# Optimization experiments

Measured on AMD Instinct MI355X. Metric: run time of the kernel, lower is better.

Reference implementation:

```python
import jax, jax.numpy as jnp
import numpy as np

B, S, D = 64, 1024, 256
N_HEADS = 1
HEAD_DIM = D // N_HEADS
MASK_VAL = -10000.0


def setup_inputs() -> dict:
    key = jax.random.key(0)
    k1, k2, k3 = jax.random.split(key, 3)
    x = jax.random.normal(k1, (B, S, D), dtype=jnp.float32)
    W_qkv = jax.random.normal(k2, (D, 3 * D), dtype=jnp.float32) * 0.02
    b_qkv = jnp.zeros((3 * D,), dtype=jnp.float32)
    W_out = jax.random.normal(k3, (D, D), dtype=jnp.float32) * 0.02
    b_out = jnp.zeros((D,), dtype=jnp.float32)
    return {"x": x, "W_qkv": W_qkv, "b_qkv": b_qkv, "W_out": W_out, "b_out": b_out}


def reference(x, W_qkv, b_qkv, W_out, b_out):
    # QKV projection: [B,S,3D]
    qkv = jnp.einsum('bsd,df->bsf', x, W_qkv) + b_qkv
    q, k, v = jnp.split(qkv, 3, axis=2)
    # split heads -> [B,H,S,hd] (H=1)
    def split_heads(t):
        return t.reshape(B, S, N_HEADS, HEAD_DIM).transpose(0, 2, 1, 3)
    q, k, v = split_heads(q), split_heads(k), split_heads(v)
    # scaled scores [B,H,S,S]
    scores = jnp.einsum('bhqd,bhkd->bhqk', q, k) / jnp.sqrt(jnp.float32(HEAD_DIM))
    causal = jnp.tril(jnp.ones((1, 1, S, S), dtype=bool))
    scores = jnp.where(causal, scores, jnp.float32(MASK_VAL))
    attn = jax.nn.softmax(scores, axis=-1)  # dropout deterministic (training=False)
    out = jnp.einsum('bhqk,bhkd->bhqd', attn, v)
    # merge heads -> [B,S,D]
    out = out.transpose(0, 2, 1, 3).reshape(B, S, D)
    out = jnp.einsum('bsd,de->bse', out, W_out) + b_out
    return out, attn
```

## Files before the change

kernel.cpp:

```cpp
#include <hip/hip_runtime.h>
#include <hip/hip_bf16.h>

#define BB 64
#define SS 1024
#define DDIM 256

typedef unsigned short u16;
typedef __attribute__((ext_vector_type(4))) float f4;
typedef __attribute__((ext_vector_type(8))) short bf16x8;
typedef __attribute__((ext_vector_type(4))) short bf16x4;
typedef __attribute__((ext_vector_type(4))) float f32x4;

__device__ inline u16 f2b(float f) {
  unsigned int u = __float_as_uint(f);
  unsigned int r = (u + 0x7fffu + ((u >> 16) & 1u)) >> 16;
  return (u16)r;
}

#define GLOAD16(g, l)                                                  \
  __builtin_amdgcn_global_load_lds(                                    \
      (const __attribute__((address_space(1))) void*)(g),              \
      (__attribute__((address_space(3))) void*)(l), 16, 0, 0)

__global__ __launch_bounds__(256) void cast_x(const float* __restrict__ x,
                                              u16* __restrict__ xb, int n8) {
  int i = blockIdx.x * 256 + threadIdx.x;
  const int stride = gridDim.x * 256;
  for (; i < n8; i += stride) {
    f4 a = ((const f4*)x)[2 * i];
    f4 b = ((const f4*)x)[2 * i + 1];
    bf16x8 o;
    o[0] = f2b(a[0]); o[1] = f2b(a[1]); o[2] = f2b(a[2]); o[3] = f2b(a[3]);
    o[4] = f2b(b[0]); o[5] = f2b(b[1]); o[6] = f2b(b[2]); o[7] = f2b(b[3]);
    ((bf16x8*)xb)[i] = o;
  }
}

__global__ __launch_bounds__(256) void cast_w(const float* __restrict__ Wqkv,
                                              const float* __restrict__ Wout,
                                              u16* __restrict__ Wqkvt,
                                              u16* __restrict__ Woutt) {
  int t = blockIdx.x * 256 + threadIdx.x;
  if (t < 256 * 768) {
    int k = t / 768, n = t % 768;
    Wqkvt[n * 256 + k] = f2b(Wqkv[t]);
  }
  if (t < 256 * 256) {
    int k = t / 256, n = t % 256;
    Woutt[n * 256 + k] = f2b(Wout[t]);
  }
}

template <int EPI, int NXT>
__global__ __launch_bounds__(256) void gemm_mfma(
    const u16* __restrict__ A, const u16* __restrict__ Bt,
    const float* __restrict__ bias, float* __restrict__ outF,
    u16* __restrict__ Qb, u16* __restrict__ Kb, u16* __restrict__ Vt) {
  __shared__ u16 As[128 * 64];
  __shared__ u16 Bs[128 * 64];
  const int t = threadIdx.x;
  const int w = t >> 6, l = t & 63;
  const int lr = l & 15, lg = l >> 4;
  const int id = blockIdx.x;
  const int r8 = id & 7;
  const int tt = id >> 3;
  const int xt = tt % NXT;
  const int yt = (tt / NXT) * 8 + r8;
  const int m0 = yt * 128, n0 = xt * 128;
  const int wm = (w >> 1) * 64, wn = (w & 1) * 64;

  f32x4 acc[4][4] = {};

  const int srow = w * 8 + (l >> 3);
  const int csrc = (l & 7) ^ (srow & 7);

  for (int k0 = 0; k0 < 256; k0 += 64) {
    __syncthreads();
#pragma unroll
    for (int i = 0; i < 4; ++i) {
      const int row = i * 32 + srow;
      GLOAD16(&A[(size_t)(m0 + row) * 256 + k0 + csrc * 8],
              &As[(i * 32 + w * 8) * 64]);
      GLOAD16(&Bt[(size_t)(n0 + row) * 256 + k0 + csrc * 8],
              &Bs[(i * 32 + w * 8) * 64]);
    }
    __syncthreads();
#pragma unroll
    for (int kc = 0; kc < 2; ++kc) {
      bf16x8 af[4], bfr[4];
#pragma unroll
      for (int f = 0; f < 4; ++f) {
        int ar = wm + f * 16 + lr;
        af[f] = *(const bf16x8*)&As[ar * 64 + (((kc * 4 + lg) ^ (ar & 7)) * 8)];
        int br = wn + f * 16 + lr;
        bfr[f] = *(const bf16x8*)&Bs[br * 64 + (((kc * 4 + lg) ^ (br & 7)) * 8)];
      }
#pragma unroll
      for (int i = 0; i < 4; ++i)
#pragma unroll
        for (int jn = 0; jn < 4; ++jn)
          acc[i][jn] = __builtin_amdgcn_mfma_f32_16x16x32_bf16(
              af[i], bfr[jn], acc[i][jn], 0, 0, 0);
    }
  }

#pragma unroll
  for (int i = 0; i < 4; ++i) {
    const int mbase = m0 + wm + i * 16 + lg * 4;
#pragma unroll
    for (int jn = 0; jn < 4; ++jn) {
      const int n = n0 + wn + jn * 16 + lr;
      const float bv = bias[n];
      if (EPI == 0) {
#pragma unroll
        for (int r = 0; r < 4; ++r)
          outF[(size_t)(mbase + r) * 256 + n] = acc[i][jn][r] + bv;
      } else {
        if (n < 256) {
#pragma unroll
          for (int r = 0; r < 4; ++r)
            Qb[(size_t)(mbase + r) * 256 + n] = f2b(acc[i][jn][r] + bv);
        } else if (n < 512) {
#pragma unroll
          for (int r = 0; r < 4; ++r)
            Kb[(size_t)(mbase + r) * 256 + (n - 256)] = f2b(acc[i][jn][r] + bv);
        } else {
          const int d = n - 512;
          const int b = mbase >> 10, sl = mbase & 1023;
          bf16x4 pk;
#pragma unroll
          for (int r = 0; r < 4; ++r) pk[r] = f2b(acc[i][jn][r] + bv);
          *(bf16x4*)&Vt[((size_t)b * 256 + d) * 1024 + sl] = pk;
        }
      }
    }
  }
}

__global__ __launch_bounds__(256) void attn_fused(
    const u16* __restrict__ Qg, const u16* __restrict__ Kg,
    const u16* __restrict__ Vtg, float* __restrict__ attn,
    u16* __restrict__ outa) {
  __shared__ u16 pool[35328];
  u16* Ks = pool;
  u16* Vs = pool + 16384;
  u16* Ps = pool + 32768;

  const int t = threadIdx.x;
  const int w = t >> 6, l = t & 63;
  const int lr = l & 15, lg = l >> 4;
  const int id = blockIdx.x;
  const int b = (id & 7) * 8 + ((id >> 3) & 7);
  const int pair = id >> 6;
  const int qta = pair, qtb = 15 - pair;
  const int d0w = w * 64;

  const u16* Kbase = Kg + (size_t)b * SS * DDIM;
  const u16* Vbase = Vtg + (size_t)b * DDIM * SS;

  auto stageK = [&](int kt, int buf) {
    const int rbase = 8 * w;
#pragma unroll
    for (int i = 0; i < 4; ++i) {
      const int rr = rbase + 2 * i + (l >> 5);
      const int chunk = l & 31;
      const int csrc = (chunk & 24) | ((chunk & 7) ^ (rr & 7));
      const u16* g = Kbase + (size_t)(kt * 32 + rr) * DDIM + csrc * 8;
      GLOAD16(g, Ks + buf * 8192 + (rbase + 2 * i) * 256);
    }
  };
  auto stageV = [&](int kt, int buf) {
    const int dbase = 64 * w;
#pragma unroll
    for (int i = 0; i < 4; ++i) {
      const int dd = dbase + 16 * i + (l >> 2);
      const u16* g = Vbase + (size_t)dd * SS + kt * 32 + (l & 3) * 8;
      GLOAD16(g, Vs + buf * 8192 + (dbase + 16 * i) * 32);
    }
  };
  auto loadQ = [&](int qt, bf16x8* qf) {
    const u16* qb = Qg + ((size_t)(b * SS + qt * 64 + w * 16 + lr)) * DDIM;
#pragma unroll
    for (int kc = 0; kc < 8; ++kc)
      qf[kc] = *(const bf16x8*)&qb[kc * 32 + lg * 8];
  };

  bf16x8 qfA[8], qfB[8];
  loadQ(qta, qfA);
  loadQ(qtb, qfB);
  const int lastA = 2 * qta + 1, lastB = 2 * qtb + 1;
  float raA[4] = {0.f, 0.f, 0.f, 0.f}, raB[4] = {0.f, 0.f, 0.f, 0.f};

  stageK(0, 0);
  __syncthreads();
  for (int kt = 0; kt <= lastB; ++kt) {
    const int buf = kt & 1;
    if (kt < lastB) stageK(kt + 1, buf ^ 1);
    const bool doA = (kt <= lastA);
#pragma unroll
    for (int sf = 0; sf < 2; ++sf) {
      const int srow = sf * 16 + lr;
      const u16* kr = Ks + buf * 8192 + srow * 256;
      f32x4 sA = {0.f, 0.f, 0.f, 0.f}, sB = {0.f, 0.f, 0.f, 0.f};
#pragma unroll
      for (int kc = 0; kc < 8; ++kc) {
        const int c = kc * 4 + lg;
        const int ch = (c & 24) | ((c & 7) ^ (srow & 7));
        bf16x8 bfr = *(const bf16x8*)&kr[ch * 8];
        sB = __builtin_amdgcn_mfma_f32_16x16x32_bf16(qfB[kc], bfr, sB, 0, 0, 0);
        if (doA)
          sA = __builtin_amdgcn_mfma_f32_16x16x32_bf16(qfA[kc], bfr, sA, 0, 0, 0);
      }
      const int scol = kt * 32 + sf * 16 + lr;
      {
        const int qrow = qtb * 64 + w * 16 + lg * 4;
#pragma unroll
        for (int r = 0; r < 4; ++r)
          raB[r] += (scol <= qrow + r) ? __expf(sB[r] * 0.0625f) : 0.f;
      }
      if (doA) {
        const int qrow = qta * 64 + w * 16 + lg * 4;
#pragma unroll
        for (int r = 0; r < 4; ++r)
          raA[r] += (scol <= qrow + r) ? __expf(sA[r] * 0.0625f) : 0.f;
      }
    }
    __syncthreads();
  }
#pragma unroll
  for (int m = 1; m < 16; m <<= 1) {
#pragma unroll
    for (int r = 0; r < 4; ++r) {
      raA[r] += __shfl_xor(raA[r], m, 64);
      raB[r] += __shfl_xor(raB[r], m, 64);
    }
  }
  float invA[4], invB[4];
#pragma unroll
  for (int r = 0; r < 4; ++r) {
    invA[r] = 1.0f / raA[r];
    invB[r] = 1.0f / raB[r];
  }

  for (int tile = 0; tile < 2; ++tile) {
    const int qt = tile ? qtb : qta;
    const int last = 2 * qt + 1;
    bf16x8 qf[8];
    loadQ(qt, qf);
    float inv[4];
#pragma unroll
    for (int r = 0; r < 4; ++r) inv[r] = tile ? invB[r] : invA[r];
    f32x4 oacc[4][4];
#pragma unroll
    for (int qb = 0; qb < 4; ++qb)
#pragma unroll
      for (int df = 0; df < 4; ++df) oacc[qb][df] = (f32x4){0.f, 0.f, 0.f, 0.f};

    float* attnw = attn + ((size_t)(b * SS + qt * 64 + w * 16)) * SS;

    __syncthreads();
    stageK(0, 0);
    stageV(0, 0);
    __syncthreads();

    for (int kt = 0; kt <= last; ++kt) {
      const int buf = kt & 1;
#pragma unroll
      for (int sf = 0; sf < 2; ++sf) {
        const int srow = sf * 16 + lr;
        const u16* kr = Ks + buf * 8192 + srow * 256;
        f32x4 s = {0.f, 0.f, 0.f, 0.f};
#pragma unroll
        for (int kc = 0; kc < 8; ++kc) {
          const int c = kc * 4 + lg;
          const int ch = (c & 24) | ((c & 7) ^ (srow & 7));
          bf16x8 bfr = *(const bf16x8*)&kr[ch * 8];
          s = __builtin_amdgcn_mfma_f32_16x16x32_bf16(qf[kc], bfr, s, 0, 0, 0);
        }
        const int scol = kt * 32 + sf * 16 + lr;
        const int qrow = qt * 64 + w * 16 + lg * 4;
#pragma unroll
        for (int r = 0; r < 4; ++r) {
          const float e = (scol <= qrow + r) ? __expf(s[r] * 0.0625f) : 0.f;
          Ps[(w * 16 + lg * 4 + r) * 40 + sf * 16 + lr] = f2b(e * inv[r]);
        }
      }
#pragma unroll
      for (int g2 = 0; g2 < 2; ++g2) {
        const int row = g2 * 8 + (l >> 3);
        const int col = (l & 7) * 4;
        bf16x4 pv = *(const bf16x4*)&Ps[(w * 16 + row) * 40 + col];
        f4 o;
#pragma unroll
        for (int j = 0; j < 4; ++j)
          o[j] = __uint_as_float(((unsigned)(u16)pv[j]) << 16);
        *(f4*)&attnw[(size_t)row * SS + kt * 32 + col] = o;
      }
      __syncthreads();
      if (kt < last) {
        stageK(kt + 1, buf ^ 1);
        stageV(kt + 1, buf ^ 1);
      }
      bf16x8 vfr[4];
      const u16* vb = Vs + buf * 8192;
#pragma unroll
      for (int df = 0; df < 4; ++df)
        vfr[df] = *(const bf16x8*)&vb[(d0w + df * 16 + lr) * 32 + lg * 8];
#pragma unroll
      for (int qb = 0; qb < 4; ++qb) {
        bf16x8 pa = *(const bf16x8*)&Ps[(qb * 16 + lr) * 40 + lg * 8];
#pragma unroll
        for (int df = 0; df < 4; ++df)
          oacc[qb][df] = __builtin_amdgcn_mfma_f32_16x16x32_bf16(
              pa, vfr[df], oacc[qb][df], 0, 0, 0);
      }
      __syncthreads();
    }

    {
      const f4 z = {0.f, 0.f, 0.f, 0.f};
      for (int c0 = (qt + 1) * 64; c0 < SS; c0 += 32) {
#pragma unroll
        for (int g2 = 0; g2 < 2; ++g2) {
          const int row = g2 * 8 + (l >> 3);
          *(f4*)&attnw[(size_t)row * SS + c0 + (l & 7) * 4] = z;
        }
      }
    }

#pragma unroll
    for (int qb = 0; qb < 4; ++qb)
#pragma unroll
      for (int df = 0; df < 4; ++df)
#pragma unroll
        for (int r = 0; r < 4; ++r)
          pool[(qb * 16 + lg * 4 + r) * 264 + d0w + df * 16 + lr] =
              f2b(oacc[qb][df][r]);
    __syncthreads();
    {
      const size_t obase = (size_t)(b * SS + qt * 64);
#pragma unroll
      for (int i = 0; i < 8; ++i) {
        const int row = w * 16 + 2 * i + (l >> 5);
        bf16x8 v = *(const bf16x8*)&pool[row * 264 + (l & 31) * 8];
        *(bf16x8*)&outa[(obase + row) * DDIM + (l & 31) * 8] = v;
      }
    }
  }
}

extern "C" void kernel_launch(void* const* d_in, const int* in_sizes, int n_in,
                              void* d_out, int out_size, void* d_ws,
                              size_t ws_size, hipStream_t stream) {
  const float* x    = (const float*)d_in[0];
  const float* Wqkv = (const float*)d_in[1];
  const float* bqkv = (const float*)d_in[2];
  const float* Wout = (const float*)d_in[3];
  const float* bout = (const float*)d_in[4];

  float* out  = (float*)d_out;
  float* attn = out + (size_t)BB * SS * DDIM;

  const size_t NTOK = (size_t)BB * SS;
  u16* ws = (u16*)d_ws;
  u16* xb    = ws;
  u16* Qb    = xb + NTOK * DDIM;
  u16* Kb    = Qb + NTOK * DDIM;
  u16* Vt    = Kb + NTOK * DDIM;
  u16* outa  = Vt + NTOK * DDIM;
  u16* Wqkvt = outa + NTOK * DDIM;
  u16* Woutt = Wqkvt + 768 * 256;

  cast_x<<<2048, 256, 0, stream>>>(x, xb, (int)(NTOK * DDIM / 8));
  cast_w<<<768, 256, 0, stream>>>(Wqkv, Wout, Wqkvt, Woutt);

  gemm_mfma<1, 6><<<3072, 256, 0, stream>>>(xb, Wqkvt, bqkv, nullptr, Qb, Kb,
                                            Vt);
  attn_fused<<<512, 256, 0, stream>>>(Qb, Kb, Vt, attn, outa);
  gemm_mfma<0, 2><<<1024, 256, 0, stream>>>(outa, Woutt, bout, out, nullptr,
                                            nullptr, nullptr);
}
```

Baseline: 266.8 us.

## Load V fragments directly from global and cut LDS for higher occupancy

Drops the V staging buffer in LDS and has each wave read its V fragments straight from global memory into registers. This roughly halves the kernel's shared memory, and launch bounds now ask for 3 blocks per CU. The __syncthreads calls are replaced with explicit vmcnt/lgkmcnt waits, raw s_barrier and sched_barrier, so each iteration needs fewer full barriers and the next K tile is staged earlier. The risks are uncoalesced strided global reads for V, register limits under the tighter launch bound, and correctness that now depends on hand-counted vmcnt values.

```diff
diff --git a/kernel.cpp b/kernel.cpp
--- a/kernel.cpp
+++ b/kernel.cpp
@@ -21,6 +21,12 @@
   __builtin_amdgcn_global_load_lds(                                    \
       (const __attribute__((address_space(1))) void*)(g),              \
       (__attribute__((address_space(3))) void*)(l), 16, 0, 0)
+
+#define WAITVM0 asm volatile("s_waitcnt vmcnt(0)" ::: "memory")
+#define WAITVM6 asm volatile("s_waitcnt vmcnt(6)" ::: "memory")
+#define LGKM0 asm volatile("s_waitcnt lgkmcnt(0)" ::: "memory")
+#define SBAR __builtin_amdgcn_s_barrier()
+#define SCHED0 __builtin_amdgcn_sched_barrier(0)
 
 __global__ __launch_bounds__(256) void cast_x(const float* __restrict__ x,
                                               u16* __restrict__ xb, int n8) {
@@ -137,14 +143,13 @@
   }
 }
 
-__global__ __launch_bounds__(256) void attn_fused(
+__global__ __launch_bounds__(256, 3) void attn_fused(
     const u16* __restrict__ Qg, const u16* __restrict__ Kg,
     const u16* __restrict__ Vtg, float* __restrict__ attn,
     u16* __restrict__ outa) {
-  __shared__ u16 pool[35328];
+  __shared__ u16 pool[18944];
   u16* Ks = pool;
-  u16* Vs = pool + 16384;
-  u16* Ps = pool + 32768;
+  u16* Ps = pool + 16384;
 
   const int t = threadIdx.x;
   const int w = t >> 6, l = t & 63;
@@ -169,15 +174,6 @@
       GLOAD16(g, Ks + buf * 8192 + (rbase + 2 * i) * 256);
     }
   };
-  auto stageV = [&](int kt, int buf) {
-    const int dbase = 64 * w;
-#pragma unroll
-    for (int i = 0; i < 4; ++i) {
-      const int dd = dbase + 16 * i + (l >> 2);
-      const u16* g = Vbase + (size_t)dd * SS + kt * 32 + (l & 3) * 8;
-      GLOAD16(g, Vs + buf * 8192 + (dbase + 16 * i) * 32);
-    }
-  };
   auto loadQ = [&](int qt, bf16x8* qf) {
     const u16* qb = Qg + ((size_t)(b * SS + qt * 64 + w * 16 + lr)) * DDIM;
 #pragma unroll
@@ -192,9 +188,11 @@
   float raA[4] = {0.f, 0.f, 0.f, 0.f}, raB[4] = {0.f, 0.f, 0.f, 0.f};
 
   stageK(0, 0);
-  __syncthreads();
   for (int kt = 0; kt <= lastB; ++kt) {
     const int buf = kt & 1;
+    WAITVM0;
+    SBAR;
+    SCHED0;
     if (kt < lastB) stageK(kt + 1, buf ^ 1);
     const bool doA = (kt <= lastA);
 #pragma unroll
@@ -225,8 +223,8 @@
           raA[r] += (scol <= qrow + r) ? __expf(sA[r] * 0.0625f) : 0.f;
       }
     }
-    __syncthreads();
-  }
+  }
+  SBAR;
 #pragma unroll
   for (int m = 1; m < 16; m <<= 1) {
 #pragma unroll
@@ -258,13 +256,20 @@
 
     float* attnw = attn + ((size_t)(b * SS + qt * 64 + w * 16)) * SS;
 
-    __syncthreads();
     stageK(0, 0);
-    stageV(0, 0);
-    __syncthreads();
+    WAITVM0;
 
     for (int kt = 0; kt <= last; ++kt) {
       const int buf = kt & 1;
+      bf16x8 vfr[4];
+#pragma unroll
+      for (int df = 0; df < 4; ++df)
+        vfr[df] = *(const bf16x8*)&Vbase[(size_t)(d0w + df * 16 + lr) * SS +
+                                         kt * 32 + lg * 8];
+      WAITVM6;
+      SBAR;
+      SCHED0;
+      if (kt < last) stageK(kt + 1, buf ^ 1);
 #pragma unroll
       for (int sf = 0; sf < 2; ++sf) {
         const int srow = sf * 16 + lr;
@@ -296,16 +301,9 @@
           o[j] = __uint_as_float(((unsigned)(u16)pv[j]) << 16);
         *(f4*)&attnw[(size_t)row * SS + kt * 32 + col] = o;
       }
-      __syncthreads();
-      if (kt < last) {
-        stageK(kt + 1, buf ^ 1);
-        stageV(kt + 1, buf ^ 1);
-      }
-      bf16x8 vfr[4];
-      const u16* vb = Vs + buf * 8192;
-#pragma unroll
-      for (int df = 0; df < 4; ++df)
-        vfr[df] = *(const bf16x8*)&vb[(d0w + df * 16 + lr) * 32 + lg * 8];
+      LGKM0;
+      SBAR;
+      SCHED0;
 #pragma unroll
       for (int qb = 0; qb < 4; ++qb) {
         bf16x8 pa = *(const bf16x8*)&Ps[(qb * 16 + lr) * 40 + lg * 8];
@@ -314,8 +312,8 @@
           oacc[qb][df] = __builtin_amdgcn_mfma_f32_16x16x32_bf16(
               pa, vfr[df], oacc[qb][df], 0, 0, 0);
       }
-      __syncthreads();
-    }
+    }
+    SBAR;
 
     {
       const f4 z = {0.f, 0.f, 0.f, 0.f};
@@ -336,7 +334,8 @@
         for (int r = 0; r < 4; ++r)
           pool[(qb * 16 + lg * 4 + r) * 264 + d0w + df * 16 + lr] =
               f2b(oacc[qb][df][r]);
-    __syncthreads();
+    LGKM0;
+    SBAR;
     {
       const size_t obase = (size_t)(b * SS + qt * 64);
 #pragma unroll
@@ -346,6 +345,7 @@
         *(bf16x8*)&outa[(obase + row) * DDIM + (l & 31) * 8] = v;
       }
     }
+    SBAR;
   }
 }
 
```

Measured after the change: 319.1 us. 19.6% more time.

## Fuse x fp32-to-bf16 cast into QKV GEMM loads and widen K tiles

Applied to the files above, without the earlier changes.

The separate cast_x kernel is removed. The QKV GEMM now reads fp32 x directly, converts it to bf16 in registers and writes it into swizzled LDS, which saves the round trip of writing and re-reading an intermediate bf16 copy of x. Separately, the attention row-sum pass stages 64-row K tiles instead of 32-row tiles, halving the loop iterations and barriers. The trade-off is that the fused A loads are now synchronous register loads rather than async global-to-LDS loads, and the larger K tiles double the LDS footprint per buffer.

```diff
diff --git a/kernel.cpp b/kernel.cpp
--- a/kernel.cpp
+++ b/kernel.cpp
@@ -21,20 +21,6 @@
   __builtin_amdgcn_global_load_lds(                                    \
       (const __attribute__((address_space(1))) void*)(g),              \
       (__attribute__((address_space(3))) void*)(l), 16, 0, 0)
-
-__global__ __launch_bounds__(256) void cast_x(const float* __restrict__ x,
-                                              u16* __restrict__ xb, int n8) {
-  int i = blockIdx.x * 256 + threadIdx.x;
-  const int stride = gridDim.x * 256;
-  for (; i < n8; i += stride) {
-    f4 a = ((const f4*)x)[2 * i];
-    f4 b = ((const f4*)x)[2 * i + 1];
-    bf16x8 o;
-    o[0] = f2b(a[0]); o[1] = f2b(a[1]); o[2] = f2b(a[2]); o[3] = f2b(a[3]);
-    o[4] = f2b(b[0]); o[5] = f2b(b[1]); o[6] = f2b(b[2]); o[7] = f2b(b[3]);
-    ((bf16x8*)xb)[i] = o;
-  }
-}
 
 __global__ __launch_bounds__(256) void cast_w(const float* __restrict__ Wqkv,
                                               const float* __restrict__ Wout,
@@ -51,11 +37,12 @@
   }
 }
 
-template <int EPI, int NXT>
+template <int EPI, int NXT, int AF32>
 __global__ __launch_bounds__(256) void gemm_mfma(
-    const u16* __restrict__ A, const u16* __restrict__ Bt,
-    const float* __restrict__ bias, float* __restrict__ outF,
-    u16* __restrict__ Qb, u16* __restrict__ Kb, u16* __restrict__ Vt) {
+    const u16* __restrict__ Ab, const float* __restrict__ Af,
+    const u16* __restrict__ Bt, const float* __restrict__ bias,
+    float* __restrict__ outF, u16* __restrict__ Qb, u16* __restrict__ Kb,
+    u16* __restrict__ Vt) {
   __shared__ u16 As[128 * 64];
   __shared__ u16 Bs[128 * 64];
   const int t = threadIdx.x;
@@ -79,10 +66,25 @@
 #pragma unroll
     for (int i = 0; i < 4; ++i) {
       const int row = i * 32 + srow;
-      GLOAD16(&A[(size_t)(m0 + row) * 256 + k0 + csrc * 8],
-              &As[(i * 32 + w * 8) * 64]);
       GLOAD16(&Bt[(size_t)(n0 + row) * 256 + k0 + csrc * 8],
               &Bs[(i * 32 + w * 8) * 64]);
+      if (AF32 == 0)
+        GLOAD16(&Ab[(size_t)(m0 + row) * 256 + k0 + csrc * 8],
+                &As[(i * 32 + w * 8) * 64]);
+    }
+    if (AF32 == 1) {
+#pragma unroll
+      for (int j = 0; j < 4; ++j) {
+        const int idx = t + j * 256;
+        const int row = idx >> 3, c = idx & 7;
+        const float* src = &Af[(size_t)(m0 + row) * 256 + k0 + c * 8];
+        f4 a0 = *(const f4*)src;
+        f4 a1 = *(const f4*)(src + 4);
+        bf16x8 o;
+        o[0] = f2b(a0[0]); o[1] = f2b(a0[1]); o[2] = f2b(a0[2]); o[3] = f2b(a0[3]);
+        o[4] = f2b(a1[0]); o[5] = f2b(a1[1]); o[6] = f2b(a1[2]); o[7] = f2b(a1[3]);
+        *(bf16x8*)&As[row * 64 + ((c ^ (row & 7)) * 8)] = o;
+      }
     }
     __syncthreads();
 #pragma unroll
@@ -158,6 +160,16 @@
   const u16* Kbase = Kg + (size_t)b * SS * DDIM;
   const u16* Vbase = Vtg + (size_t)b * DDIM * SS;
 
+  auto stageK64 = [&](int kt, int buf) {
+#pragma unroll
+    for (int i = 0; i < 8; ++i) {
+      const int rr = 16 * w + 2 * i + (l >> 5);
+      const int chunk = l & 31;
+      const int csrc = (chunk & 24) | ((chunk & 7) ^ (rr & 7));
+      const u16* g = Kbase + (size_t)(kt * 64 + rr) * DDIM + csrc * 8;
+      GLOAD16(g, pool + buf * 16384 + (16 * w + 2 * i) * 256);
+    }
+  };
   auto stageK = [&](int kt, int buf) {
     const int rbase = 8 * w;
 #pragma unroll
@@ -188,19 +200,18 @@
   bf16x8 qfA[8], qfB[8];
   loadQ(qta, qfA);
   loadQ(qtb, qfB);
-  const int lastA = 2 * qta + 1, lastB = 2 * qtb + 1;
   float raA[4] = {0.f, 0.f, 0.f, 0.f}, raB[4] = {0.f, 0.f, 0.f, 0.f};
 
-  stageK(0, 0);
+  stageK64(0, 0);
   __syncthreads();
-  for (int kt = 0; kt <= lastB; ++kt) {
+  for (int kt = 0; kt <= qtb; ++kt) {
     const int buf = kt & 1;
-    if (kt < lastB) stageK(kt + 1, buf ^ 1);
-    const bool doA = (kt <= lastA);
-#pragma unroll
-    for (int sf = 0; sf < 2; ++sf) {
+    if (kt < qtb) stageK64(kt + 1, buf ^ 1);
+    const bool doA = (kt <= qta);
+#pragma unroll
+    for (int sf = 0; sf < 4; ++sf) {
       const int srow = sf * 16 + lr;
-      const u16* kr = Ks + buf * 8192 + srow * 256;
+      const u16* kr = pool + buf * 16384 + srow * 256;
       f32x4 sA = {0.f, 0.f, 0.f, 0.f}, sB = {0.f, 0.f, 0.f, 0.f};
 #pragma unroll
       for (int kc = 0; kc < 8; ++kc) {
@@ -211,7 +222,7 @@
         if (doA)
           sA = __builtin_amdgcn_mfma_f32_16x16x32_bf16(qfA[kc], bfr, sA, 0, 0, 0);
       }
-      const int scol = kt * 32 + sf * 16 + lr;
+      const int scol = kt * 64 + sf * 16 + lr;
       {
         const int qrow = qtb * 64 + w * 16 + lg * 4;
 #pragma unroll
@@ -363,20 +374,18 @@
 
   const size_t NTOK = (size_t)BB * SS;
   u16* ws = (u16*)d_ws;
-  u16* xb    = ws;
-  u16* Qb    = xb + NTOK * DDIM;
+  u16* Qb    = ws;
   u16* Kb    = Qb + NTOK * DDIM;
   u16* Vt    = Kb + NTOK * DDIM;
   u16* outa  = Vt + NTOK * DDIM;
   u16* Wqkvt = outa + NTOK * DDIM;
   u16* Woutt = Wqkvt + 768 * 256;
 
-  cast_x<<<2048, 256, 0, stream>>>(x, xb, (int)(NTOK * DDIM / 8));
   cast_w<<<768, 256, 0, stream>>>(Wqkv, Wout, Wqkvt, Woutt);
 
-  gemm_mfma<1, 6><<<3072, 256, 0, stream>>>(xb, Wqkvt, bqkv, nullptr, Qb, Kb,
-                                            Vt);
+  gemm_mfma<1, 6, 1><<<3072, 256, 0, stream>>>(nullptr, x, Wqkvt, bqkv,
+                                               nullptr, Qb, Kb, Vt);
   attn_fused<<<512, 256, 0, stream>>>(Qb, Kb, Vt, attn, outa);
-  gemm_mfma<0, 2><<<1024, 256, 0, stream>>>(outa, Woutt, bout, out, nullptr,
-                                            nullptr, nullptr);
-}
+  gemm_mfma<0, 2, 0><<<1024, 256, 0, stream>>>(outa, nullptr, Woutt, bout, out,
+                                               nullptr, nullptr, nullptr);
+}
```

Result: slower. 273.2 us (+2.4%).
